# Kernel tuning notes

Measured on AMD Instinct MI355X. Metric: run time of the kernel, lower is better.

Reference implementation:

```python
import jax, jax.numpy as jnp
import numpy as np

S_STATES, C_TYPES, G_GENES = 16, 64, 20000


def setup_inputs() -> dict:
    key = jax.random.key(0)
    k1, k2, k3, k4 = jax.random.split(key, 4)
    Z_mu = jax.random.normal(k1, (C_TYPES, G_GENES), dtype=jnp.float32)
    # positive log-normal sigmas, moderate scale for numerical stability
    Z_sigma = jax.random.uniform(k2, (C_TYPES, G_GENES), dtype=jnp.float32) * 0.5 + 0.1
    # build a valid correlation matrix (PSD with unit diagonal) so var >= 0
    L = jax.random.normal(k3, (C_TYPES, C_TYPES), dtype=jnp.float32)
    cov = L @ L.T + C_TYPES * jnp.eye(C_TYPES, dtype=jnp.float32)
    d = jnp.sqrt(jnp.diag(cov))
    corr = cov / (d[:, None] * d[None, :])
    # cell_prob rows on the simplex (Dirichlet-like), per state
    cell_prob = jax.nn.softmax(jax.random.normal(k4, (S_STATES, C_TYPES), dtype=jnp.float32), axis=1)
    return {"Z_mu": Z_mu, "Z_sigma": Z_sigma, "corr": corr, "cell_prob": cell_prob}


def reference(Z_mu, Z_sigma, corr, cell_prob):
    """Vectorized LogNorm.calculate_mu_sigma.

    Z_mu, Z_sigma: (C, G); corr: (C, C); cell_prob: (S, C).
    Returns mu, sigma of shape (S, G) -- moment-matched log-normal sum params
    for every (state, gene) pair, matching the nested-loop torch original.
    """
    # EV[s,c,g] = exp(mu + sigma^2/2) * w  (first moment of each component, weighted)
    ev_base = jnp.exp(Z_mu + 0.5 * Z_sigma ** 2)            # (C, G)
    EV = cell_prob[:, :, None] * ev_base[None, :, :]         # (S, C, G)
    Ssum = EV.sum(axis=1)                                    # (S, G)
    # A[s,c,g] = EV * sigma; var = sum_{c,d} A_c corr_{cd} A_d / Ssum^2
    A = EV * Z_sigma[None, :, :]                             # (S, C, G)
    var = jnp.einsum('scg,cd,sdg->sg', A, corr, A) / (Ssum ** 2)  # (S, G)
    mu_s = jnp.log(Ssum) - 0.5 * var
    sigma_s = jnp.sqrt(var)
    return (mu_s, sigma_s)
```

## Files before the change

kernel.cpp:

```cpp
#include <hip/hip_runtime.h>


#define S_STATES 16
#define C_TYPES  64
#define G_GENES  20000
#define OUT_HALF (S_STATES * G_GENES)
#define NPAIR    96
#define PER_WAVE 24

typedef _Float16 f16x2 __attribute__((ext_vector_type(2)));
typedef _Float16 f16x8 __attribute__((ext_vector_type(8)));
typedef float    f32x4 __attribute__((ext_vector_type(4)));

union Frag8 { f16x2 p[4]; f16x8 v; uint4 u; _Float16 h[8]; };

__global__ __launch_bounds__(64)
void build_A(const float* __restrict__ corr, const float* __restrict__ w,
             unsigned short* __restrict__ cwA)
{
    const int p    = blockIdx.x;
    const int lane = threadIdx.x;
    const int gl   = lane & 15;
    const int q    = lane >> 4;
    Frag8 v;
    if (p < NPAIR) {
        const int dh = (p >= 64);
        const int c  = dh ? p - 32 : p;
        const int d0 = dh * 32 + q * 8;
        const float wc = w[gl * C_TYPES + c];
        const float4 c0 = *(const float4*)(corr + c * C_TYPES + d0);
        const float4 c1 = *(const float4*)(corr + c * C_TYPES + d0 + 4);
        const float4 w0 = *(const float4*)(w + gl * C_TYPES + d0);
        const float4 w1 = *(const float4*)(w + gl * C_TYPES + d0 + 4);
        const float cv[8] = {c0.x,c0.y,c0.z,c0.w,c1.x,c1.y,c1.z,c1.w};
        const float wv[8] = {w0.x,w0.y,w0.z,w0.w,w1.x,w1.y,w1.z,w1.w};
#pragma unroll
        for (int j = 0; j < 8; ++j) {
            const int d = d0 + j;
            const float sc = (d < c) ? 2.0f : (d == c ? 1.0f : 0.0f);
            v.h[j] = (_Float16)(sc * cv[j] * wc * wv[j]);
        }
    } else {
        const int k0 = (p - NPAIR) * 32 + q * 8;
        const float4 w0 = *(const float4*)(w + gl * C_TYPES + k0);
        const float4 w1 = *(const float4*)(w + gl * C_TYPES + k0 + 4);
        const float wv[8] = {w0.x,w0.y,w0.z,w0.w,w1.x,w1.y,w1.z,w1.w};
#pragma unroll
        for (int j = 0; j < 8; ++j) v.h[j] = (_Float16)wv[j];
    }
    *(uint4*)(cwA + (p << 9) + lane * 8) = v.u;
}

__global__ __launch_bounds__(256, 3)
void lognorm_main(const float* __restrict__ Z_mu,
                  const float* __restrict__ Z_sigma,
                  const unsigned short* __restrict__ cwA,
                  float* __restrict__ out)
{
    __shared__ f16x2 x2pT[32][35];
    __shared__ f16x2 x1pT[32][35];
    __shared__ f16x2 x2tp[C_TYPES][21];
    __shared__ float accs[4][S_STATES][33];
    __shared__ float ssum_s[S_STATES][33];

    const int gt    = blockIdx.x;
    const int tid   = threadIdx.x;
    const int w     = tid >> 6;
    const int lane  = tid & 63;
    const int gl    = lane & 15;
    const int q     = lane >> 4;
    const int gbase = gt * 32;

    Frag8 afr[PER_WAVE];
    {
        const unsigned short* Abase = cwA + (w << 9) + lane * 8;
#pragma unroll
        for (int i = 0; i < PER_WAVE; ++i)
            afr[i].u = *(const uint4*)(Abase + (i << 11));
    }
    Frag8 wf0, wf1;
    if (w < 2) {
        wf0.u = *(const uint4*)(cwA + ((NPAIR + 0) << 9) + lane * 8);
        wf1.u = *(const uint4*)(cwA + ((NPAIR + 1) << 9) + lane * 8);
    }

    {
        const int dp = tid >> 3;
        const int gq = tid & 7;
        const int ga = gq * 2;
        const float* zm0 = Z_mu    + (2*dp) * G_GENES + gbase + ga;
        const float* zs0 = Z_sigma + (2*dp) * G_GENES + gbase + ga;
        const float2 m00 = *(const float2*)zm0;
        const float2 m01 = *(const float2*)(zm0 + 16);
        const float2 m10 = *(const float2*)(zm0 + G_GENES);
        const float2 m11 = *(const float2*)(zm0 + G_GENES + 16);
        const float2 s00 = *(const float2*)zs0;
        const float2 s01 = *(const float2*)(zs0 + 16);
        const float2 s10 = *(const float2*)(zs0 + G_GENES);
        const float2 s11 = *(const float2*)(zs0 + G_GENES + 16);
        float x1v[2][2][2], x2v[2][2][2];
#define XDO(r,h,j,M,S) { const float s_=(S); const float e_=__expf(fmaf(0.5f*s_,s_,(M)))*0.25f; \
                         x1v[r][h][j]=e_; x2v[r][h][j]=e_*s_; }
        XDO(0,0,0, m00.x, s00.x) XDO(0,0,1, m00.y, s00.y)
        XDO(0,1,0, m01.x, s01.x) XDO(0,1,1, m01.y, s01.y)
        XDO(1,0,0, m10.x, s10.x) XDO(1,0,1, m10.y, s10.y)
        XDO(1,1,0, m11.x, s11.x) XDO(1,1,1, m11.y, s11.y)
#undef XDO
#pragma unroll
        for (int h = 0; h < 2; ++h)
#pragma unroll
            for (int j = 0; j < 2; ++j) {
                const int g = ga + j + 16 * h;
                f16x2 a, b;
                a.x = (_Float16)x2v[0][h][j]; a.y = (_Float16)x2v[1][h][j];
                b.x = (_Float16)x1v[0][h][j]; b.y = (_Float16)x1v[1][h][j];
                x2pT[g][dp] = a;
                x1pT[g][dp] = b;
            }
#pragma unroll
        for (int r = 0; r < 2; ++r)
#pragma unroll
            for (int j = 0; j < 2; ++j) {
                f16x2 a;
                a.x = (_Float16)x2v[r][0][j];
                a.y = (_Float16)x2v[r][1][j];
                x2tp[2*dp + r][ga + j] = a;
            }
    }
    __syncthreads();

    f16x2 xh[2][4][2];
#pragma unroll
    for (int dh = 0; dh < 2; ++dh)
#pragma unroll
        for (int t = 0; t < 2; ++t)
#pragma unroll
            for (int jp = 0; jp < 4; ++jp)
                xh[dh][jp][t] = x2pT[gl + 16*t][dh*16 + q*4 + jp];

    f32x4 acc0 = {0.f,0.f,0.f,0.f}, acc1 = {0.f,0.f,0.f,0.f};
#pragma unroll
    for (int i = 0; i < PER_WAVE; ++i) {
        const int c  = i*4 + w - ((i >= 16) ? 32 : 0);
        const int dh = (i >= 16) ? 1 : 0;
        const f16x2 xct = x2tp[c][gl];
        Frag8 b0, b1;
#pragma unroll
        for (int jp = 0; jp < 4; ++jp) {
            f16x2 s0; s0.x = xct.x; s0.y = xct.x;
            f16x2 s1; s1.x = xct.y; s1.y = xct.y;
            b0.p[jp] = s0 * xh[dh][jp][0];
            b1.p[jp] = s1 * xh[dh][jp][1];
        }
        acc0 = __builtin_amdgcn_mfma_f32_16x16x32_f16(afr[i].v, b0.v, acc0, 0, 0, 0);
        acc1 = __builtin_amdgcn_mfma_f32_16x16x32_f16(afr[i].v, b1.v, acc1, 0, 0, 0);
    }
#pragma unroll
    for (int r = 0; r < 4; ++r) {
        accs[w][q*4 + r][gl]      = acc0[r];
        accs[w][q*4 + r][gl + 16] = acc1[r];
    }

    if (w < 2) {
        Frag8 x1f[2];
#pragma unroll
        for (int kk = 0; kk < 2; ++kk)
#pragma unroll
            for (int jp = 0; jp < 4; ++jp)
                x1f[kk].p[jp] = x1pT[gl + 16*w][kk*16 + q*4 + jp];
        f32x4 sa = {0.f,0.f,0.f,0.f};
        sa = __builtin_amdgcn_mfma_f32_16x16x32_f16(wf0.v, x1f[0].v, sa, 0, 0, 0);
        sa = __builtin_amdgcn_mfma_f32_16x16x32_f16(wf1.v, x1f[1].v, sa, 0, 0, 0);
#pragma unroll
        for (int r = 0; r < 4; ++r) ssum_s[q*4 + r][gl + 16*w] = sa[r];
    }
    __syncthreads();

    const int s  = tid >> 4;
    const int gx = tid & 15;
#pragma unroll
    for (int t = 0; t < 2; ++t) {
        const int gg = gx + 16 * t;
        const float vn = (accs[0][s][gg] + accs[1][s][gg])
                       + (accs[2][s][gg] + accs[3][s][gg]);
        const float ss   = ssum_s[s][gg];
        const float rvar = fmaxf(vn, 0.f) / (ss * ss);
        out[s * G_GENES + gbase + gg] =
            __logf(ss) + 1.3862943611f - 0.5f * rvar;
        out[OUT_HALF + s * G_GENES + gbase + gg] = sqrtf(rvar);
    }
}

extern "C" void kernel_launch(void* const* d_in, const int* in_sizes, int n_in,
                              void* d_out, int out_size, void* d_ws, size_t ws_size,
                              hipStream_t stream) {
    const float* Z_mu      = (const float*)d_in[0];
    const float* Z_sigma   = (const float*)d_in[1];
    const float* corr      = (const float*)d_in[2];
    const float* cell_prob = (const float*)d_in[3];
    float* out = (float*)d_out;
    unsigned short* cwA = (unsigned short*)d_ws;

    build_A<<<dim3(NPAIR + 2), dim3(64), 0, stream>>>(corr, cell_prob, cwA);

    const int gtiles = G_GENES / 32;
    lognorm_main<<<dim3(gtiles), dim3(256), 0, stream>>>(
        Z_mu, Z_sigma, cwA, out);
}
```

Before: 16.59 us.

## Halve gene tile to 16 and stream A fragments from memory

```diff
diff --git a/kernel.cpp b/kernel.cpp
--- a/kernel.cpp
+++ b/kernel.cpp
@@ -51,17 +51,16 @@
     *(uint4*)(cwA + (p << 9) + lane * 8) = v.u;
 }
 
-__global__ __launch_bounds__(256, 3)
+__global__ __launch_bounds__(256, 4)
 void lognorm_main(const float* __restrict__ Z_mu,
                   const float* __restrict__ Z_sigma,
                   const unsigned short* __restrict__ cwA,
                   float* __restrict__ out)
 {
-    __shared__ f16x2 x2pT[32][35];
-    __shared__ f16x2 x1pT[32][35];
-    __shared__ f16x2 x2tp[C_TYPES][21];
-    __shared__ float accs[4][S_STATES][33];
-    __shared__ float ssum_s[S_STATES][33];
+    __shared__ f16x2 x2pT[16][35];
+    __shared__ f16x2 x1pT[16][35];
+    __shared__ float accs[4][S_STATES][17];
+    __shared__ float ssum_s[S_STATES][17];
 
     const int gt    = blockIdx.x;
     const int tid   = threadIdx.x;
@@ -69,126 +68,88 @@
     const int lane  = tid & 63;
     const int gl    = lane & 15;
     const int q     = lane >> 4;
-    const int gbase = gt * 32;
+    const int gbase = gt * 16;
 
-    Frag8 afr[PER_WAVE];
-    {
-        const unsigned short* Abase = cwA + (w << 9) + lane * 8;
-#pragma unroll
-        for (int i = 0; i < PER_WAVE; ++i)
-            afr[i].u = *(const uint4*)(Abase + (i << 11));
-    }
     Frag8 wf0, wf1;
-    if (w < 2) {
+    if (w == 0) {
         wf0.u = *(const uint4*)(cwA + ((NPAIR + 0) << 9) + lane * 8);
         wf1.u = *(const uint4*)(cwA + ((NPAIR + 1) << 9) + lane * 8);
     }
 
     {
-        const int dp = tid >> 3;
-        const int gq = tid & 7;
-        const int ga = gq * 2;
-        const float* zm0 = Z_mu    + (2*dp) * G_GENES + gbase + ga;
-        const float* zs0 = Z_sigma + (2*dp) * G_GENES + gbase + ga;
-        const float2 m00 = *(const float2*)zm0;
-        const float2 m01 = *(const float2*)(zm0 + 16);
-        const float2 m10 = *(const float2*)(zm0 + G_GENES);
-        const float2 m11 = *(const float2*)(zm0 + G_GENES + 16);
-        const float2 s00 = *(const float2*)zs0;
-        const float2 s01 = *(const float2*)(zs0 + 16);
-        const float2 s10 = *(const float2*)(zs0 + G_GENES);
-        const float2 s11 = *(const float2*)(zs0 + G_GENES + 16);
-        float x1v[2][2][2], x2v[2][2][2];
-#define XDO(r,h,j,M,S) { const float s_=(S); const float e_=__expf(fmaf(0.5f*s_,s_,(M)))*0.25f; \
-                         x1v[r][h][j]=e_; x2v[r][h][j]=e_*s_; }
-        XDO(0,0,0, m00.x, s00.x) XDO(0,0,1, m00.y, s00.y)
-        XDO(0,1,0, m01.x, s01.x) XDO(0,1,1, m01.y, s01.y)
-        XDO(1,0,0, m10.x, s10.x) XDO(1,0,1, m10.y, s10.y)
-        XDO(1,1,0, m11.x, s11.x) XDO(1,1,1, m11.y, s11.y)
-#undef XDO
+        const int gx  = tid & 15;
+        const int dpA = tid >> 4;
 #pragma unroll
-        for (int h = 0; h < 2; ++h)
-#pragma unroll
-            for (int j = 0; j < 2; ++j) {
-                const int g = ga + j + 16 * h;
-                f16x2 a, b;
-                a.x = (_Float16)x2v[0][h][j]; a.y = (_Float16)x2v[1][h][j];
-                b.x = (_Float16)x1v[0][h][j]; b.y = (_Float16)x1v[1][h][j];
-                x2pT[g][dp] = a;
-                x1pT[g][dp] = b;
-            }
-#pragma unroll
-        for (int r = 0; r < 2; ++r)
-#pragma unroll
-            for (int j = 0; j < 2; ++j) {
-                f16x2 a;
-                a.x = (_Float16)x2v[r][0][j];
-                a.y = (_Float16)x2v[r][1][j];
-                x2tp[2*dp + r][ga + j] = a;
-            }
+        for (int t = 0; t < 2; ++t) {
+            const int dp = dpA + 16 * t;
+            const float m0 = Z_mu   [(2*dp)     * G_GENES + gbase + gx];
+            const float m1 = Z_mu   [(2*dp + 1) * G_GENES + gbase + gx];
+            const float s0 = Z_sigma[(2*dp)     * G_GENES + gbase + gx];
+            const float s1 = Z_sigma[(2*dp + 1) * G_GENES + gbase + gx];
+            const float e0 = __expf(fmaf(0.5f * s0, s0, m0)) * 0.25f;
+            const float e1 = __expf(fmaf(0.5f * s1, s1, m1)) * 0.25f;
+            f16x2 a, b;
+            a.x = (_Float16)(e0 * s0); a.y = (_Float16)(e1 * s1);
+            b.x = (_Float16)e0;        b.y = (_Float16)e1;
+            x2pT[gx][dp] = a;
+            x1pT[gx][dp] = b;
+        }
     }
     __syncthreads();
 
-    f16x2 xh[2][4][2];
+    f16x2 xh[2][4];
 #pragma unroll
     for (int dh = 0; dh < 2; ++dh)
 #pragma unroll
-        for (int t = 0; t < 2; ++t)
-#pragma unroll
-            for (int jp = 0; jp < 4; ++jp)
-                xh[dh][jp][t] = x2pT[gl + 16*t][dh*16 + q*4 + jp];
+        for (int jp = 0; jp < 4; ++jp)
+            xh[dh][jp] = x2pT[gl][dh * 16 + q * 4 + jp];
 
+    const unsigned short* Abase = cwA + (w << 9) + lane * 8;
+    const int wq = w >> 1;
+    const int wc = w & 1;
     f32x4 acc0 = {0.f,0.f,0.f,0.f}, acc1 = {0.f,0.f,0.f,0.f};
 #pragma unroll
     for (int i = 0; i < PER_WAVE; ++i) {
-        const int c  = i*4 + w - ((i >= 16) ? 32 : 0);
+        Frag8 af; af.u = *(const uint4*)(Abase + (i << 11));
         const int dh = (i >= 16) ? 1 : 0;
-        const f16x2 xct = x2tp[c][gl];
-        Frag8 b0, b1;
+        const int dp = 2*i - dh*16 + wq;
+        const f16x2 pr = x2pT[gl][dp];
+        const _Float16 xc = wc ? pr.y : pr.x;
+        f16x2 s; s.x = xc; s.y = xc;
+        Frag8 b;
+#pragma unroll
+        for (int jp = 0; jp < 4; ++jp) b.p[jp] = s * xh[dh][jp];
+        if (i & 1) acc1 = __builtin_amdgcn_mfma_f32_16x16x32_f16(af.v, b.v, acc1, 0, 0, 0);
+        else       acc0 = __builtin_amdgcn_mfma_f32_16x16x32_f16(af.v, b.v, acc0, 0, 0, 0);
+    }
+    const f32x4 acc = acc0 + acc1;
+#pragma unroll
+    for (int r = 0; r < 4; ++r) accs[w][q*4 + r][gl] = acc[r];
+
+    if (w == 0) {
+        Frag8 x1f0, x1f1;
 #pragma unroll
         for (int jp = 0; jp < 4; ++jp) {
-            f16x2 s0; s0.x = xct.x; s0.y = xct.x;
-            f16x2 s1; s1.x = xct.y; s1.y = xct.y;
-            b0.p[jp] = s0 * xh[dh][jp][0];
-            b1.p[jp] = s1 * xh[dh][jp][1];
+            x1f0.p[jp] = x1pT[gl][q*4 + jp];
+            x1f1.p[jp] = x1pT[gl][16 + q*4 + jp];
         }
-        acc0 = __builtin_amdgcn_mfma_f32_16x16x32_f16(afr[i].v, b0.v, acc0, 0, 0, 0);
-        acc1 = __builtin_amdgcn_mfma_f32_16x16x32_f16(afr[i].v, b1.v, acc1, 0, 0, 0);
-    }
+        f32x4 sa = {0.f,0.f,0.f,0.f};
+        sa = __builtin_amdgcn_mfma_f32_16x16x32_f16(wf0.v, x1f0.v, sa, 0, 0, 0);
+        sa = __builtin_amdgcn_mfma_f32_16x16x32_f16(wf1.v, x1f1.v, sa, 0, 0, 0);
 #pragma unroll
-    for (int r = 0; r < 4; ++r) {
-        accs[w][q*4 + r][gl]      = acc0[r];
-        accs[w][q*4 + r][gl + 16] = acc1[r];
-    }
-
-    if (w < 2) {
-        Frag8 x1f[2];
-#pragma unroll
-        for (int kk = 0; kk < 2; ++kk)
-#pragma unroll
-            for (int jp = 0; jp < 4; ++jp)
-                x1f[kk].p[jp] = x1pT[gl + 16*w][kk*16 + q*4 + jp];
-        f32x4 sa = {0.f,0.f,0.f,0.f};
-        sa = __builtin_amdgcn_mfma_f32_16x16x32_f16(wf0.v, x1f[0].v, sa, 0, 0, 0);
-        sa = __builtin_amdgcn_mfma_f32_16x16x32_f16(wf1.v, x1f[1].v, sa, 0, 0, 0);
-#pragma unroll
-        for (int r = 0; r < 4; ++r) ssum_s[q*4 + r][gl + 16*w] = sa[r];
+        for (int r = 0; r < 4; ++r) ssum_s[q*4 + r][gl] = sa[r];
     }
     __syncthreads();
 
     const int s  = tid >> 4;
     const int gx = tid & 15;
-#pragma unroll
-    for (int t = 0; t < 2; ++t) {
-        const int gg = gx + 16 * t;
-        const float vn = (accs[0][s][gg] + accs[1][s][gg])
-                       + (accs[2][s][gg] + accs[3][s][gg]);
-        const float ss   = ssum_s[s][gg];
-        const float rvar = fmaxf(vn, 0.f) / (ss * ss);
-        out[s * G_GENES + gbase + gg] =
-            __logf(ss) + 1.3862943611f - 0.5f * rvar;
-        out[OUT_HALF + s * G_GENES + gbase + gg] = sqrtf(rvar);
-    }
+    const float vn = (accs[0][s][gx] + accs[1][s][gx])
+                   + (accs[2][s][gx] + accs[3][s][gx]);
+    const float ss   = ssum_s[s][gx];
+    const float rvar = fmaxf(vn, 0.f) / (ss * ss);
+    out[s * G_GENES + gbase + gx] =
+        __logf(ss) + 1.3862943611f - 0.5f * rvar;
+    out[OUT_HALF + s * G_GENES + gbase + gx] = sqrtf(rvar);
 }
 
 extern "C" void kernel_launch(void* const* d_in, const int* in_sizes, int n_in,
@@ -203,7 +164,7 @@
 
     build_A<<<dim3(NPAIR + 2), dim3(64), 0, stream>>>(corr, cell_prob, cwA);
 
-    const int gtiles = G_GENES / 32;
+    const int gtiles = G_GENES / 16;
     lognorm_main<<<dim3(gtiles), dim3(256), 0, stream>>>(
         Z_mu, Z_sigma, cwA, out);
 }
```

After: 16.82 us. No clear change (+1.4%).

## Fuse A-matrix construction into main kernel, drop separate build_A launch

Applied to the files above, without the earlier changes.

```diff
diff --git a/kernel.cpp b/kernel.cpp
--- a/kernel.cpp
+++ b/kernel.cpp
@@ -5,7 +5,6 @@
 #define C_TYPES  64
 #define G_GENES  20000
 #define OUT_HALF (S_STATES * G_GENES)
-#define NPAIR    96
 #define PER_WAVE 24
 
 typedef _Float16 f16x2 __attribute__((ext_vector_type(2)));
@@ -14,49 +13,14 @@
 
 union Frag8 { f16x2 p[4]; f16x8 v; uint4 u; _Float16 h[8]; };
 
-__global__ __launch_bounds__(64)
-void build_A(const float* __restrict__ corr, const float* __restrict__ w,
-             unsigned short* __restrict__ cwA)
+__global__ __launch_bounds__(256, 3)
+void lognorm_fused(const float* __restrict__ Z_mu,
+                   const float* __restrict__ Z_sigma,
+                   const float* __restrict__ corr,
+                   const float* __restrict__ w,
+                   float* __restrict__ out)
 {
-    const int p    = blockIdx.x;
-    const int lane = threadIdx.x;
-    const int gl   = lane & 15;
-    const int q    = lane >> 4;
-    Frag8 v;
-    if (p < NPAIR) {
-        const int dh = (p >= 64);
-        const int c  = dh ? p - 32 : p;
-        const int d0 = dh * 32 + q * 8;
-        const float wc = w[gl * C_TYPES + c];
-        const float4 c0 = *(const float4*)(corr + c * C_TYPES + d0);
-        const float4 c1 = *(const float4*)(corr + c * C_TYPES + d0 + 4);
-        const float4 w0 = *(const float4*)(w + gl * C_TYPES + d0);
-        const float4 w1 = *(const float4*)(w + gl * C_TYPES + d0 + 4);
-        const float cv[8] = {c0.x,c0.y,c0.z,c0.w,c1.x,c1.y,c1.z,c1.w};
-        const float wv[8] = {w0.x,w0.y,w0.z,w0.w,w1.x,w1.y,w1.z,w1.w};
-#pragma unroll
-        for (int j = 0; j < 8; ++j) {
-            const int d = d0 + j;
-            const float sc = (d < c) ? 2.0f : (d == c ? 1.0f : 0.0f);
-            v.h[j] = (_Float16)(sc * cv[j] * wc * wv[j]);
-        }
-    } else {
-        const int k0 = (p - NPAIR) * 32 + q * 8;
-        const float4 w0 = *(const float4*)(w + gl * C_TYPES + k0);
-        const float4 w1 = *(const float4*)(w + gl * C_TYPES + k0 + 4);
-        const float wv[8] = {w0.x,w0.y,w0.z,w0.w,w1.x,w1.y,w1.z,w1.w};
-#pragma unroll
-        for (int j = 0; j < 8; ++j) v.h[j] = (_Float16)wv[j];
-    }
-    *(uint4*)(cwA + (p << 9) + lane * 8) = v.u;
-}
-
-__global__ __launch_bounds__(256, 3)
-void lognorm_main(const float* __restrict__ Z_mu,
-                  const float* __restrict__ Z_sigma,
-                  const unsigned short* __restrict__ cwA,
-                  float* __restrict__ out)
-{
+    __shared__ _Float16 mcorr[C_TYPES][C_TYPES];
     __shared__ f16x2 x2pT[32][35];
     __shared__ f16x2 x1pT[32][35];
     __shared__ f16x2 x2tp[C_TYPES][21];
@@ -65,39 +29,64 @@
 
     const int gt    = blockIdx.x;
     const int tid   = threadIdx.x;
-    const int w     = tid >> 6;
+    const int w4    = tid >> 6;
     const int lane  = tid & 63;
     const int gl    = lane & 15;
     const int q     = lane >> 4;
     const int gbase = gt * 32;
 
-    Frag8 afr[PER_WAVE];
+    const int dp_x = tid >> 3;
+    const int ga_x = (tid & 7) * 2;
+    const float* zm0 = Z_mu    + (2*dp_x) * G_GENES + gbase + ga_x;
+    const float* zs0 = Z_sigma + (2*dp_x) * G_GENES + gbase + ga_x;
+    const float2 m00 = *(const float2*)zm0;
+    const float2 m01 = *(const float2*)(zm0 + 16);
+    const float2 m10 = *(const float2*)(zm0 + G_GENES);
+    const float2 m11 = *(const float2*)(zm0 + G_GENES + 16);
+    const float2 s00 = *(const float2*)zs0;
+    const float2 s01 = *(const float2*)(zs0 + 16);
+    const float2 s10 = *(const float2*)(zs0 + G_GENES);
+    const float2 s11 = *(const float2*)(zs0 + G_GENES + 16);
+
     {
-        const unsigned short* Abase = cwA + (w << 9) + lane * 8;
-#pragma unroll
-        for (int i = 0; i < PER_WAVE; ++i)
-            afr[i].u = *(const uint4*)(Abase + (i << 11));
-    }
-    Frag8 wf0, wf1;
-    if (w < 2) {
-        wf0.u = *(const uint4*)(cwA + ((NPAIR + 0) << 9) + lane * 8);
-        wf1.u = *(const uint4*)(cwA + ((NPAIR + 1) << 9) + lane * 8);
-    }
+        const int c   = tid >> 2;
+        const int b0c = (tid & 3) * 16;
+        const float* crow = corr + c * C_TYPES + b0c;
+        const float4 c0 = *(const float4*)(crow);
+        const float4 c1 = *(const float4*)(crow + 4);
+        const float4 c2 = *(const float4*)(crow + 8);
+        const float4 c3 = *(const float4*)(crow + 12);
+        const float cv[16] = {c0.x,c0.y,c0.z,c0.w, c1.x,c1.y,c1.z,c1.w,
+                              c2.x,c2.y,c2.z,c2.w, c3.x,c3.y,c3.z,c3.w};
+        Frag8 f0, f1;
+#pragma unroll
+        for (int jj = 0; jj < 8; ++jj) {
+            const int d0 = b0c + jj, d1 = b0c + 8 + jj;
+            const float sc0 = (d0 < c) ? 2.f : (d0 == c ? 1.f : 0.f);
+            const float sc1 = (d1 < c) ? 2.f : (d1 == c ? 1.f : 0.f);
+            f0.h[jj] = (_Float16)(sc0 * cv[jj]);
+            f1.h[jj] = (_Float16)(sc1 * cv[8 + jj]);
+        }
+        *(uint4*)&mcorr[c][b0c]     = f0.u;
+        *(uint4*)&mcorr[c][b0c + 8] = f1.u;
+    }
+
+    Frag8 wd16[2];
+#pragma unroll
+    for (int dh = 0; dh < 2; ++dh) {
+        const float4 a = *(const float4*)(w + gl * C_TYPES + dh * 32 + q * 8);
+        const float4 b = *(const float4*)(w + gl * C_TYPES + dh * 32 + q * 8 + 4);
+        wd16[dh].h[0] = (_Float16)a.x; wd16[dh].h[1] = (_Float16)a.y;
+        wd16[dh].h[2] = (_Float16)a.z; wd16[dh].h[3] = (_Float16)a.w;
+        wd16[dh].h[4] = (_Float16)b.x; wd16[dh].h[5] = (_Float16)b.y;
+        wd16[dh].h[6] = (_Float16)b.z; wd16[dh].h[7] = (_Float16)b.w;
+    }
+    _Float16 wc16[16];
+#pragma unroll
+    for (int k = 0; k < 16; ++k)
+        wc16[k] = (_Float16)w[gl * C_TYPES + 4 * k + w4];
 
     {
-        const int dp = tid >> 3;
-        const int gq = tid & 7;
-        const int ga = gq * 2;
-        const float* zm0 = Z_mu    + (2*dp) * G_GENES + gbase + ga;
-        const float* zs0 = Z_sigma + (2*dp) * G_GENES + gbase + ga;
-        const float2 m00 = *(const float2*)zm0;
-        const float2 m01 = *(const float2*)(zm0 + 16);
-        const float2 m10 = *(const float2*)(zm0 + G_GENES);
-        const float2 m11 = *(const float2*)(zm0 + G_GENES + 16);
-        const float2 s00 = *(const float2*)zs0;
-        const float2 s01 = *(const float2*)(zs0 + 16);
-        const float2 s10 = *(const float2*)(zs0 + G_GENES);
-        const float2 s11 = *(const float2*)(zs0 + G_GENES + 16);
         float x1v[2][2][2], x2v[2][2][2];
 #define XDO(r,h,j,M,S) { const float s_=(S); const float e_=__expf(fmaf(0.5f*s_,s_,(M)))*0.25f; \
                          x1v[r][h][j]=e_; x2v[r][h][j]=e_*s_; }
@@ -110,12 +99,12 @@
         for (int h = 0; h < 2; ++h)
 #pragma unroll
             for (int j = 0; j < 2; ++j) {
-                const int g = ga + j + 16 * h;
+                const int g = ga_x + j + 16 * h;
                 f16x2 a, b;
                 a.x = (_Float16)x2v[0][h][j]; a.y = (_Float16)x2v[1][h][j];
                 b.x = (_Float16)x1v[0][h][j]; b.y = (_Float16)x1v[1][h][j];
-                x2pT[g][dp] = a;
-                x1pT[g][dp] = b;
+                x2pT[g][dp_x] = a;
+                x1pT[g][dp_x] = b;
             }
 #pragma unroll
         for (int r = 0; r < 2; ++r)
@@ -124,7 +113,7 @@
                 f16x2 a;
                 a.x = (_Float16)x2v[r][0][j];
                 a.y = (_Float16)x2v[r][1][j];
-                x2tp[2*dp + r][ga + j] = a;
+                x2tp[2*dp_x + r][ga_x + j] = a;
             }
     }
     __syncthreads();
@@ -141,38 +130,45 @@
     f32x4 acc0 = {0.f,0.f,0.f,0.f}, acc1 = {0.f,0.f,0.f,0.f};
 #pragma unroll
     for (int i = 0; i < PER_WAVE; ++i) {
-        const int c  = i*4 + w - ((i >= 16) ? 32 : 0);
-        const int dh = (i >= 16) ? 1 : 0;
+        const int dh  = (i >= 16) ? 1 : 0;
+        const int c   = i*4 + w4 - dh*32;
+        const int idx = dh ? (i - 8) : i;
+        Frag8 mc; mc.u = *(const uint4*)&mcorr[c][dh*32 + q*8];
+        f16x2 wcp; wcp.x = wc16[idx]; wcp.y = wc16[idx];
+        Frag8 af;
+#pragma unroll
+        for (int jp = 0; jp < 4; ++jp)
+            af.p[jp] = (mc.p[jp] * wd16[dh].p[jp]) * wcp;
         const f16x2 xct = x2tp[c][gl];
+        f16x2 s0; s0.x = xct.x; s0.y = xct.x;
+        f16x2 s1; s1.x = xct.y; s1.y = xct.y;
         Frag8 b0, b1;
 #pragma unroll
         for (int jp = 0; jp < 4; ++jp) {
-            f16x2 s0; s0.x = xct.x; s0.y = xct.x;
-            f16x2 s1; s1.x = xct.y; s1.y = xct.y;
             b0.p[jp] = s0 * xh[dh][jp][0];
             b1.p[jp] = s1 * xh[dh][jp][1];
         }
-        acc0 = __builtin_amdgcn_mfma_f32_16x16x32_f16(afr[i].v, b0.v, acc0, 0, 0, 0);
-        acc1 = __builtin_amdgcn_mfma_f32_16x16x32_f16(afr[i].v, b1.v, acc1, 0, 0, 0);
+        acc0 = __builtin_amdgcn_mfma_f32_16x16x32_f16(af.v, b0.v, acc0, 0, 0, 0);
+        acc1 = __builtin_amdgcn_mfma_f32_16x16x32_f16(af.v, b1.v, acc1, 0, 0, 0);
     }
 #pragma unroll
     for (int r = 0; r < 4; ++r) {
-        accs[w][q*4 + r][gl]      = acc0[r];
-        accs[w][q*4 + r][gl + 16] = acc1[r];
-    }
-
-    if (w < 2) {
+        accs[w4][q*4 + r][gl]      = acc0[r];
+        accs[w4][q*4 + r][gl + 16] = acc1[r];
+    }
+
+    if (w4 < 2) {
         Frag8 x1f[2];
 #pragma unroll
         for (int kk = 0; kk < 2; ++kk)
 #pragma unroll
             for (int jp = 0; jp < 4; ++jp)
-                x1f[kk].p[jp] = x1pT[gl + 16*w][kk*16 + q*4 + jp];
+                x1f[kk].p[jp] = x1pT[gl + 16*w4][kk*16 + q*4 + jp];
         f32x4 sa = {0.f,0.f,0.f,0.f};
-        sa = __builtin_amdgcn_mfma_f32_16x16x32_f16(wf0.v, x1f[0].v, sa, 0, 0, 0);
-        sa = __builtin_amdgcn_mfma_f32_16x16x32_f16(wf1.v, x1f[1].v, sa, 0, 0, 0);
-#pragma unroll
-        for (int r = 0; r < 4; ++r) ssum_s[q*4 + r][gl + 16*w] = sa[r];
+        sa = __builtin_amdgcn_mfma_f32_16x16x32_f16(wd16[0].v, x1f[0].v, sa, 0, 0, 0);
+        sa = __builtin_amdgcn_mfma_f32_16x16x32_f16(wd16[1].v, x1f[1].v, sa, 0, 0, 0);
+#pragma unroll
+        for (int r = 0; r < 4; ++r) ssum_s[q*4 + r][gl + 16*w4] = sa[r];
     }
     __syncthreads();
 
@@ -199,11 +195,8 @@
     const float* corr      = (const float*)d_in[2];
     const float* cell_prob = (const float*)d_in[3];
     float* out = (float*)d_out;
-    unsigned short* cwA = (unsigned short*)d_ws;
-
-    build_A<<<dim3(NPAIR + 2), dim3(64), 0, stream>>>(corr, cell_prob, cwA);
 
     const int gtiles = G_GENES / 32;
-    lognorm_main<<<dim3(gtiles), dim3(256), 0, stream>>>(
-        Z_mu, Z_sigma, cwA, out);
+    lognorm_fused<<<dim3(gtiles), dim3(256), 0, stream>>>(
+        Z_mu, Z_sigma, corr, cell_prob, out);
 }
```

After: 16.52 us. Within noise of the previous version (-0.4%).
